# Optimization experiments

Hardware: AMD Instinct MI355X
Metric: run time of the kernel (lower is better)

## Reference

```python
import jax, jax.numpy as jnp
import numpy as np
import math

N_LEVELS = 16
F_PER_LEVEL = 2
LOG2_T = 19
T = 1 << LOG2_T
BASE_RES = 16
MAX_RES = 2048
PER_LEVEL_SCALE = (MAX_RES / BASE_RES) ** (1.0 / (N_LEVELS - 1))
BOUND = 0.5
PRIMES = (np.uint32(1), np.uint32(2654435761), np.uint32(805459861))


def _weight_norm(v, g):
    # w = g * v / ||v||_row (torch weight_norm over dim=1)
    return v * (g / jnp.linalg.norm(v, axis=1))[:, None]


def _softplus100(x):
    # torch Softplus(beta=100)
    return jax.nn.softplus(100.0 * x) * 0.01


def hashgrid_encode(x01, table):
    # x01: [N,3] in [0,1]; table: [L, T, F]
    feats = []
    for l in range(N_LEVELS):
        scale = BASE_RES * (PER_LEVEL_SCALE ** l) - 1.0  # tcnn grid scale
        res = int(math.ceil(scale)) + 1
        pos = x01 * scale + 0.5
        pos_floor = jnp.floor(pos)
        w = pos - pos_floor                      # [N,3] trilinear fracs
        c0 = pos_floor.astype(jnp.uint32)        # [N,3] base corner
        dense = (res ** 3) <= T                  # static per level
        acc = jnp.zeros((x01.shape[0], F_PER_LEVEL), dtype=table.dtype)
        for corner in range(8):
            off = [(corner >> d) & 1 for d in range(3)]
            cx = c0[:, 0] + np.uint32(off[0])
            cy = c0[:, 1] + np.uint32(off[1])
            cz = c0[:, 2] + np.uint32(off[2])
            if dense:
                idx = cx + cy * np.uint32(res) + cz * np.uint32(res * res)
            else:
                idx = (cx * PRIMES[0]) ^ (cy * PRIMES[1]) ^ (cz * PRIMES[2])
                idx = idx & np.uint32(T - 1)
            wc = ((w[:, 0] if off[0] else 1.0 - w[:, 0])
                  * (w[:, 1] if off[1] else 1.0 - w[:, 1])
                  * (w[:, 2] if off[2] else 1.0 - w[:, 2]))
            acc = acc + wc[:, None] * table[l, idx.astype(jnp.int32)]
        feats.append(acc)
    return jnp.concatenate(feats, axis=-1)  # [N, 32]


def setup_inputs() -> dict:
    key = jax.random.key(0)
    ks = jax.random.split(key, 4)
    N = 2 ** 21
    x = jax.random.uniform(ks[0], (N, 3), jnp.float32, -BOUND, BOUND)
    table = jax.random.uniform(ks[1], (N_LEVELS, T, F_PER_LEVEL), jnp.float32, -1e-4, 1e-4)
    d_in, d_hid, d_out = 35, 64, 13
    v1 = jax.random.normal(ks[2], (d_hid, d_in), jnp.float32) * (math.sqrt(2) / math.sqrt(d_hid))
    v2 = jax.random.normal(ks[3], (d_out, d_hid), jnp.float32) * 1e-4 + math.sqrt(math.pi) / math.sqrt(d_hid)
    g1 = jnp.linalg.norm(v1, axis=1)
    g2 = jnp.linalg.norm(v2, axis=1)
    b1 = jnp.zeros((d_hid,), jnp.float32)
    b2 = jnp.full((d_out,), -0.5, jnp.float32)  # -sphere_init_radius
    return {"x": x, "table": table, "v1": v1, "g1": g1, "b1": b1,
            "v2": v2, "g2": g2, "b2": b2}


def reference(x, table, v1, g1, b1, v2, g2, b2):
    x01 = jnp.clip((x + BOUND) / (2.0 * BOUND), 0.0, 1.0)
    enc = hashgrid_encode(x01, table)            # [N, 32]
    h = jnp.concatenate([x, enc], axis=1)        # [N, 35]
    w1 = _weight_norm(v1, g1)
    w2 = _weight_norm(v2, g2)
    h = _softplus100(h @ w1.T + b1)
    out = h @ w2.T + b2                          # [N, 13]
    return out
```

## Files before the change

kernel.cpp:

```cpp
#include <hip/hip_runtime.h>
#include <hip/hip_fp16.h>
#include <cstdint>
#include <cmath>

#define NLEV 16
#define NHASH 11
#define NDENSE 5
#define TBL (1u << 19)

struct LevelParams {
    float scale[NLEV];
    uint32_t res[NLEV];
    uint32_t hashed_mask;
};

__global__ __launch_bounds__(128) void prep_weights(
    const float* __restrict__ v1, const float* __restrict__ g1,
    const float* __restrict__ v2, const float* __restrict__ g2,
    float* __restrict__ w1t, float* __restrict__ w2n)
{
    int t = threadIdx.x;
    if (t < 64) {
        float s = 0.f;
        #pragma unroll
        for (int k = 0; k < 35; ++k) { float v = v1[t*35 + k]; s += v*v; }
        float f = g1[t] / sqrtf(s);
        #pragma unroll
        for (int k = 0; k < 35; ++k) w1t[k*64 + t] = v1[t*35 + k] * f;
    } else if (t < 77) {
        int r = t - 64;
        float s = 0.f;
        #pragma unroll
        for (int k = 0; k < 64; ++k) { float v = v2[r*64 + k]; s += v*v; }
        float f = g2[r] / sqrtf(s);
        #pragma unroll
        for (int k = 0; k < 64; ++k) w2n[r*64 + k] = v2[r*64 + k] * f;
    }
}

__global__ __launch_bounds__(256) void pack_table(
    const float2* __restrict__ in, uint32_t* __restrict__ out, int n)
{
    int i = blockIdx.x * 256 + threadIdx.x;
    if (i < n) {
        float2 v = in[i];
        __half2 h = __floats2half2_rn(v.x, v.y);
        out[i] = *reinterpret_cast<uint32_t*>(&h);
    }
}

__device__ __forceinline__ void encode_one(
    float u0, float u1, float u2, float s, uint32_t res, bool hashed,
    const uint32_t* __restrict__ tl, float& a0, float& a1)
{
    float px = u0 * s + 0.5f;
    float py = u1 * s + 0.5f;
    float pz = u2 * s + 0.5f;
    float fx = floorf(px), fy = floorf(py), fz = floorf(pz);
    float wx1 = px - fx, wy1 = py - fy, wz1 = pz - fz;
    float wx0 = 1.f - wx1, wy0 = 1.f - wy1, wz0 = 1.f - wz1;
    uint32_t cx = (uint32_t)fx, cy = (uint32_t)fy, cz = (uint32_t)fz;

    uint32_t ix0, ix1, iy0, iy1, iz0, iz1;
    if (hashed) {
        ix0 = cx;                 ix1 = cx + 1u;
        iy0 = cy * 2654435761u;   iy1 = (cy + 1u) * 2654435761u;
        iz0 = cz * 805459861u;    iz1 = (cz + 1u) * 805459861u;
    } else {
        ix0 = cx;                 ix1 = cx + 1u;
        iy0 = cy * res;           iy1 = iy0 + res;
        uint32_t rr = res * res;
        iz0 = cz * rr;            iz1 = iz0 + rr;
    }

    uint32_t idxs[8];
    #pragma unroll
    for (int c = 0; c < 8; ++c) {
        uint32_t jx = (c & 1) ? ix1 : ix0;
        uint32_t jy = (c & 2) ? iy1 : iy0;
        uint32_t jz = (c & 4) ? iz1 : iz0;
        idxs[c] = hashed ? ((jx ^ jy ^ jz) & (TBL - 1u)) : (jx + jy + jz);
    }
    uint32_t raw[8];
    #pragma unroll
    for (int c = 0; c < 8; ++c) raw[c] = tl[idxs[c]];

    float wxy00 = wx0*wy0, wxy10 = wx1*wy0, wxy01 = wx0*wy1, wxy11 = wx1*wy1;
    a0 = 0.f; a1 = 0.f;
    #pragma unroll
    for (int c = 0; c < 8; ++c) {
        float wxy = (c & 2) ? ((c & 1) ? wxy11 : wxy01)
                            : ((c & 1) ? wxy10 : wxy00);
        float w = wxy * ((c & 4) ? wz1 : wz0);
        __half2 hv = *reinterpret_cast<__half2*>(&raw[c]);
        float2 v = __half22float2(hv);
        a0 += w * v.x;
        a1 += w * v.y;
    }
}

__global__ __launch_bounds__(256) void encode_hashed(
    const float* __restrict__ x, const uint32_t* __restrict__ tpk,
    uint32_t* __restrict__ feats, int N, int chunks_per_level, LevelParams P)
{
    int bid = blockIdx.x;
    int li = bid / chunks_per_level;
    int l = li + NDENSE;
    int base = (bid - li * chunks_per_level) * 512 + threadIdx.x;
    const uint32_t* tl = tpk + (size_t)l * TBL;
    float s = P.scale[l];

    int p[2] = { base, base + 256 };

    uint2 Q[2][4];
    uint32_t par[2];
    float wx0[2], wx1[2], wyz[2][4];

    #pragma unroll
    for (int t = 0; t < 2; ++t) {
        int pp = (p[t] < N) ? p[t] : (N - 1);
        float x0 = __builtin_nontemporal_load(&x[3*(size_t)pp + 0]);
        float x1 = __builtin_nontemporal_load(&x[3*(size_t)pp + 1]);
        float x2 = __builtin_nontemporal_load(&x[3*(size_t)pp + 2]);
        float u0 = fminf(fmaxf(x0 + 0.5f, 0.f), 1.f);
        float u1 = fminf(fmaxf(x1 + 0.5f, 0.f), 1.f);
        float u2 = fminf(fmaxf(x2 + 0.5f, 0.f), 1.f);

        float px = u0 * s + 0.5f;
        float py = u1 * s + 0.5f;
        float pz = u2 * s + 0.5f;
        float fx = floorf(px), fy = floorf(py), fz = floorf(pz);
        float a1f = px - fx, b1f = py - fy, c1f = pz - fz;
        wx1[t] = a1f; wx0[t] = 1.f - a1f;
        float wy0 = 1.f - b1f, wz0 = 1.f - c1f;
        uint32_t cx = (uint32_t)fx, cy = (uint32_t)fy, cz = (uint32_t)fz;

        wyz[t][0] = wy0 * wz0;
        wyz[t][1] = b1f * wz0;
        wyz[t][2] = wy0 * c1f;
        wyz[t][3] = b1f * c1f;

        uint32_t hy0 = cy * 2654435761u, hy1 = (cy + 1u) * 2654435761u;
        uint32_t hz0 = cz * 805459861u,  hz1 = (cz + 1u) * 805459861u;
        uint32_t r[4] = { hy0 ^ hz0, hy1 ^ hz0, hy0 ^ hz1, hy1 ^ hz1 };

        par[t] = 0u;
        if (!(cx & 1u)) {
            #pragma unroll
            for (int k = 0; k < 4; ++k) {
                uint32_t v0 = (cx ^ r[k]) & (TBL - 1u);
                Q[t][k] = *reinterpret_cast<const uint2*>(tl + (v0 & ~1u));
                par[t] |= (v0 & 1u) << k;
            }
        } else {
            #pragma unroll
            for (int k = 0; k < 4; ++k) {
                uint32_t v0 = (cx ^ r[k]) & (TBL - 1u);
                uint32_t v1 = ((cx + 1u) ^ r[k]) & (TBL - 1u);
                Q[t][k].x = tl[v0];
                Q[t][k].y = tl[v1];
            }
        }
    }

    #pragma unroll
    for (int t = 0; t < 2; ++t) {
        float a0 = 0.f, a1 = 0.f;
        #pragma unroll
        for (int k = 0; k < 4; ++k) {
            uint32_t swap = (par[t] >> k) & 1u;
            uint32_t b0 = swap ? Q[t][k].y : Q[t][k].x;
            uint32_t b1 = swap ? Q[t][k].x : Q[t][k].y;
            __half2 h0 = *reinterpret_cast<__half2*>(&b0);
            __half2 h1 = *reinterpret_cast<__half2*>(&b1);
            float2 c0 = __half22float2(h0);
            float2 c1 = __half22float2(h1);
            a0 += wyz[t][k] * (wx0[t] * c0.x + wx1[t] * c1.x);
            a1 += wyz[t][k] * (wx0[t] * c0.y + wx1[t] * c1.y);
        }
        __half2 hv = __floats2half2_rn(a0, a1);
        if (p[t] < N) {
            __builtin_nontemporal_store(*reinterpret_cast<uint32_t*>(&hv),
                                        &feats[(size_t)li * N + p[t]]);
        }
    }
}

__global__ __launch_bounds__(256) void mlp_dense(
    const float* __restrict__ x, const uint32_t* __restrict__ tpk,
    const uint32_t* __restrict__ feats,
    const float* __restrict__ w1t,
    const float* __restrict__ b1,
    const float* __restrict__ w2,
    const float* __restrict__ b2,
    float* __restrict__ out, int N, LevelParams P)
{
    int p = blockIdx.x * 256 + threadIdx.x;
    bool valid = (p < N);
    int pp = valid ? p : (N - 1);

    float x0 = x[3*(size_t)pp + 0];
    float x1 = x[3*(size_t)pp + 1];
    float x2 = x[3*(size_t)pp + 2];
    float u0 = fminf(fmaxf(x0 + 0.5f, 0.f), 1.f);
    float u1 = fminf(fmaxf(x1 + 0.5f, 0.f), 1.f);
    float u2 = fminf(fmaxf(x2 + 0.5f, 0.f), 1.f);

    uint32_t rf[NHASH];
    #pragma unroll
    for (int li = 0; li < NHASH; ++li) rf[li] = feats[(size_t)li * N + pp];

    float h[64];
    #pragma unroll
    for (int j = 0; j < 64; ++j) {
        h[j] = b1[j] + x0 * w1t[0*64 + j] + x1 * w1t[1*64 + j] + x2 * w1t[2*64 + j];
    }

    #pragma unroll
    for (int l = 0; l < NDENSE; ++l) {
        const uint32_t* tl = tpk + (size_t)l * TBL;
        float a0, a1;
        encode_one(u0, u1, u2, P.scale[l], P.res[l], false, tl, a0, a1);
        const float* c0p = w1t + (3 + 2*l) * 64;
        const float* c1p = c0p + 64;
        #pragma unroll
        for (int j = 0; j < 64; ++j) h[j] += a0 * c0p[j] + a1 * c1p[j];
    }

    #pragma unroll
    for (int li = 0; li < NHASH; ++li) {
        __half2 hv = *reinterpret_cast<__half2*>(&rf[li]);
        float2 f = __half22float2(hv);
        int l = li + NDENSE;
        const float* c0p = w1t + (3 + 2*l) * 64;
        const float* c1p = c0p + 64;
        #pragma unroll
        for (int j = 0; j < 64; ++j) h[j] += f.x * c0p[j] + f.y * c1p[j];
    }

    #pragma unroll
    for (int j = 0; j < 64; ++j) {
        float z = 100.f * h[j];
        float t = __expf(-fabsf(z));
        h[j] = (fmaxf(z, 0.f) + __logf(1.f + t)) * 0.01f;
    }

    float* op = out + (size_t)pp * 13;
    for (int o = 0; o < 13; ++o) {
        float a = b2[o];
        const float* wr = w2 + o * 64;
        #pragma unroll
        for (int k = 0; k < 64; ++k) a = fmaf(h[k], wr[k], a);
        if (valid) op[o] = a;
    }
}

template <int PACKED>
__global__ __launch_bounds__(256) void sdf_fused(
    const float* __restrict__ x, const void* __restrict__ table,
    const float* __restrict__ w1t, const float* __restrict__ b1,
    const float* __restrict__ w2, const float* __restrict__ b2,
    float* __restrict__ out, int N, LevelParams P)
{
    int i = blockIdx.x * 256 + threadIdx.x;
    bool valid = (i < N);
    int ii = valid ? i : (N - 1);

    float x0 = x[3*(size_t)ii + 0];
    float x1 = x[3*(size_t)ii + 1];
    float x2 = x[3*(size_t)ii + 2];
    float u0 = fminf(fmaxf(x0 + 0.5f, 0.f), 1.f);
    float u1 = fminf(fmaxf(x1 + 0.5f, 0.f), 1.f);
    float u2 = fminf(fmaxf(x2 + 0.5f, 0.f), 1.f);

    float h[64];
    #pragma unroll
    for (int j = 0; j < 64; ++j) {
        h[j] = b1[j] + x0 * w1t[0*64 + j] + x1 * w1t[1*64 + j] + x2 * w1t[2*64 + j];
    }

    for (int l = 0; l < NLEV; ++l) {
        bool hashed = (P.hashed_mask >> l) & 1u;
        float a0, a1;
        if (PACKED) {
            const uint32_t* tl = (const uint32_t*)table + (size_t)l * TBL;
            encode_one(u0, u1, u2, P.scale[l], P.res[l], hashed, tl, a0, a1);
        } else {
            const float* tl = (const float*)table + (size_t)l * (size_t)(TBL * 2u);
            float s = P.scale[l]; uint32_t res = P.res[l];
            float px = u0*s + 0.5f, py = u1*s + 0.5f, pz = u2*s + 0.5f;
            float fx = floorf(px), fy = floorf(py), fz = floorf(pz);
            float wx1 = px-fx, wy1 = py-fy, wz1 = pz-fz;
            float wx0 = 1.f-wx1, wy0 = 1.f-wy1, wz0 = 1.f-wz1;
            uint32_t cx = (uint32_t)fx, cy = (uint32_t)fy, cz = (uint32_t)fz;
            a0 = 0.f; a1 = 0.f;
            #pragma unroll
            for (int c = 0; c < 8; ++c) {
                uint32_t jx = cx + (c & 1);
                uint32_t jy = cy + ((c >> 1) & 1);
                uint32_t jz = cz + ((c >> 2) & 1);
                uint32_t idx = hashed
                    ? ((jx ^ (jy * 2654435761u) ^ (jz * 805459861u)) & (TBL - 1u))
                    : (jx + jy * res + jz * res * res);
                float w = ((c & 1) ? wx1 : wx0) * ((c & 2) ? wy1 : wy0)
                        * ((c & 4) ? wz1 : wz0);
                float2 v = *reinterpret_cast<const float2*>(tl + (size_t)idx * 2u);
                a0 += w * v.x; a1 += w * v.y;
            }
        }
        const float* c0p = w1t + (3 + 2*l) * 64;
        const float* c1p = c0p + 64;
        #pragma unroll
        for (int j = 0; j < 64; ++j) h[j] += a0 * c0p[j] + a1 * c1p[j];
    }

    #pragma unroll
    for (int j = 0; j < 64; ++j) {
        float z = 100.f * h[j];
        float t = __expf(-fabsf(z));
        h[j] = (fmaxf(z, 0.f) + __logf(1.f + t)) * 0.01f;
    }

    float* op = out + (size_t)ii * 13;
    for (int o = 0; o < 13; ++o) {
        float a = b2[o];
        const float* wr = w2 + o * 64;
        #pragma unroll
        for (int k = 0; k < 64; ++k) a += h[k] * wr[k];
        if (valid) op[o] = a;
    }
}

extern "C" void kernel_launch(void* const* d_in, const int* in_sizes, int n_in,
                              void* d_out, int out_size, void* d_ws, size_t ws_size,
                              hipStream_t stream)
{
    const float* x     = (const float*)d_in[0];
    const float* table = (const float*)d_in[1];
    const float* v1    = (const float*)d_in[2];
    const float* g1    = (const float*)d_in[3];
    const float* b1    = (const float*)d_in[4];
    const float* v2    = (const float*)d_in[5];
    const float* g2    = (const float*)d_in[6];
    const float* b2    = (const float*)d_in[7];
    float* out = (float*)d_out;
    int N = in_sizes[0] / 3;

    const int n_entries = NLEV * (int)TBL;
    const size_t packed_bytes = (size_t)n_entries * 4u;
    const size_t feats_bytes  = (size_t)NHASH * (size_t)N * 4u;
    const size_t w_bytes = (35*64 + 13*64) * sizeof(float);

    bool two_pass  = (ws_size >= packed_bytes + feats_bytes + w_bytes);
    bool packed_ok = (ws_size >= packed_bytes + w_bytes);

    uint32_t* tpk   = (uint32_t*)d_ws;
    uint32_t* feats = (uint32_t*)((char*)d_ws + packed_bytes);
    size_t w_off = packed_ok ? (packed_bytes + (two_pass ? feats_bytes : 0)) : 0;
    float* w1t = (float*)((char*)d_ws + w_off);
    float* w2n = w1t + 35 * 64;

    LevelParams P;
    P.hashed_mask = 0u;
    double pls = pow(128.0, 1.0 / 15.0);
    for (int l = 0; l < NLEV; ++l) {
        double sc = 16.0 * pow(pls, (double)l) - 1.0;
        P.scale[l] = (float)sc;
        uint32_t res = (uint32_t)(ceil(sc)) + 1u;
        P.res[l] = res;
        uint64_t r3 = (uint64_t)res * res * res;
        if (r3 > (uint64_t)TBL) P.hashed_mask |= (1u << l);
    }

    prep_weights<<<1, 128, 0, stream>>>(v1, g1, v2, g2, w1t, w2n);

    int chunks = (N + 255) / 256;
    if (two_pass) {
        pack_table<<<(n_entries + 255) / 256, 256, 0, stream>>>(
            (const float2*)table, tpk, n_entries);
        int chunks2 = (N + 511) / 512;
        encode_hashed<<<chunks2 * NHASH, 256, 0, stream>>>(
            x, tpk, feats, N, chunks2, P);
        mlp_dense<<<chunks, 256, 0, stream>>>(
            x, tpk, feats, w1t, b1, w2n, b2, out, N, P);
    } else if (packed_ok) {
        pack_table<<<(n_entries + 255) / 256, 256, 0, stream>>>(
            (const float2*)table, tpk, n_entries);
        sdf_fused<1><<<chunks, 256, 0, stream>>>(
            x, (const void*)tpk, w1t, b1, w2n, b2, out, N, P);
    } else {
        sdf_fused<0><<<chunks, 256, 0, stream>>>(
            x, (const void*)table, w1t, b1, w2n, b2, out, N, P);
    }
}
```

Baseline: 780.5 us.

## Spatially bucket-sort points before hash-grid encoding to improve gather locality

Adds a counting sort of points into a 32^3 spatial grid (histogram, scan, atomic scatter) that writes packed float4 coordinates with the original index. The encode and MLP kernels then read the sorted points, and outputs are scattered back to their original positions. The aim is to make table gathers from neighbouring threads hit nearby entries so cache hit rates improve for the random uniform inputs. In exchange it adds extra kernels, global atomics, a 32 MB sorted buffer and scattered output writes, and it runs only when the workspace is large enough.

```diff
diff --git a/kernel.cpp b/kernel.cpp
--- a/kernel.cpp
+++ b/kernel.cpp
@@ -7,6 +7,7 @@
 #define NHASH 11
 #define NDENSE 5
 #define TBL (1u << 19)
+#define NBKT 32768
 
 struct LevelParams {
     float scale[NLEV];
@@ -46,6 +47,75 @@
         float2 v = in[i];
         __half2 h = __floats2half2_rn(v.x, v.y);
         out[i] = *reinterpret_cast<uint32_t*>(&h);
+    }
+}
+
+__device__ __forceinline__ uint32_t bucket_key(float u0, float u1, float u2)
+{
+    uint32_t a = min(31u, (uint32_t)(u0 * 32.f));
+    uint32_t b = min(31u, (uint32_t)(u1 * 32.f));
+    uint32_t c = min(31u, (uint32_t)(u2 * 32.f));
+    return (a << 10) | (b << 5) | c;
+}
+
+__device__ __forceinline__ void load_u(const float* __restrict__ x, int pp,
+                                       float& u0, float& u1, float& u2)
+{
+    float x0 = x[3*(size_t)pp + 0];
+    float x1 = x[3*(size_t)pp + 1];
+    float x2 = x[3*(size_t)pp + 2];
+    u0 = fminf(fmaxf(x0 + 0.5f, 0.f), 1.f);
+    u1 = fminf(fmaxf(x1 + 0.5f, 0.f), 1.f);
+    u2 = fminf(fmaxf(x2 + 0.5f, 0.f), 1.f);
+}
+
+__global__ __launch_bounds__(256) void hist_kernel(
+    const float* __restrict__ x, uint32_t* __restrict__ hist, int N)
+{
+    int i = blockIdx.x * 256 + threadIdx.x;
+    if (i < N) {
+        float u0, u1, u2;
+        load_u(x, i, u0, u1, u2);
+        atomicAdd(&hist[bucket_key(u0, u1, u2)], 1u);
+    }
+}
+
+__global__ __launch_bounds__(1024) void scan_hist(
+    const uint32_t* __restrict__ hist, uint32_t* __restrict__ offs)
+{
+    __shared__ uint32_t part[1024];
+    int t = threadIdx.x;
+    uint32_t loc[32];
+    uint32_t s = 0;
+    #pragma unroll
+    for (int k = 0; k < 32; ++k) { loc[k] = s; s += hist[t*32 + k]; }
+    part[t] = s;
+    __syncthreads();
+    for (int d = 1; d < 1024; d <<= 1) {
+        uint32_t v = (t >= d) ? part[t - d] : 0u;
+        __syncthreads();
+        part[t] += v;
+        __syncthreads();
+    }
+    uint32_t base = (t > 0) ? part[t - 1] : 0u;
+    #pragma unroll
+    for (int k = 0; k < 32; ++k) offs[t*32 + k] = base + loc[k];
+}
+
+__global__ __launch_bounds__(256) void scatter_kernel(
+    const float* __restrict__ x, uint32_t* __restrict__ offs,
+    float4* __restrict__ xs4, int N)
+{
+    int i = blockIdx.x * 256 + threadIdx.x;
+    if (i < N) {
+        float x0 = x[3*(size_t)i + 0];
+        float x1 = x[3*(size_t)i + 1];
+        float x2 = x[3*(size_t)i + 2];
+        float u0 = fminf(fmaxf(x0 + 0.5f, 0.f), 1.f);
+        float u1 = fminf(fmaxf(x1 + 0.5f, 0.f), 1.f);
+        float u2 = fminf(fmaxf(x2 + 0.5f, 0.f), 1.f);
+        uint32_t pos = atomicAdd(&offs[bucket_key(u0, u1, u2)], 1u);
+        xs4[pos] = make_float4(x0, x1, x2, __int_as_float(i));
     }
 }
 
@@ -99,8 +169,10 @@
     }
 }
 
+template <int SORTED>
 __global__ __launch_bounds__(256) void encode_hashed(
-    const float* __restrict__ x, const uint32_t* __restrict__ tpk,
+    const float* __restrict__ x, const float4* __restrict__ xs4,
+    const uint32_t* __restrict__ tpk,
     uint32_t* __restrict__ feats, int N, int chunks_per_level, LevelParams P)
 {
     int bid = blockIdx.x;
@@ -119,12 +191,15 @@
     #pragma unroll
     for (int t = 0; t < 2; ++t) {
         int pp = (p[t] < N) ? p[t] : (N - 1);
-        float x0 = __builtin_nontemporal_load(&x[3*(size_t)pp + 0]);
-        float x1 = __builtin_nontemporal_load(&x[3*(size_t)pp + 1]);
-        float x2 = __builtin_nontemporal_load(&x[3*(size_t)pp + 2]);
-        float u0 = fminf(fmaxf(x0 + 0.5f, 0.f), 1.f);
-        float u1 = fminf(fmaxf(x1 + 0.5f, 0.f), 1.f);
-        float u2 = fminf(fmaxf(x2 + 0.5f, 0.f), 1.f);
+        float u0, u1, u2;
+        if (SORTED) {
+            float4 v4 = xs4[pp];
+            u0 = fminf(fmaxf(v4.x + 0.5f, 0.f), 1.f);
+            u1 = fminf(fmaxf(v4.y + 0.5f, 0.f), 1.f);
+            u2 = fminf(fmaxf(v4.z + 0.5f, 0.f), 1.f);
+        } else {
+            load_u(x, pp, u0, u1, u2);
+        }
 
         float px = u0 * s + 0.5f;
         float py = u1 * s + 0.5f;
@@ -186,8 +261,10 @@
     }
 }
 
+template <int SORTED>
 __global__ __launch_bounds__(256) void mlp_dense(
-    const float* __restrict__ x, const uint32_t* __restrict__ tpk,
+    const float* __restrict__ x, const float4* __restrict__ xs4,
+    const uint32_t* __restrict__ tpk,
     const uint32_t* __restrict__ feats,
     const float* __restrict__ w1t,
     const float* __restrict__ b1,
@@ -199,9 +276,18 @@
     bool valid = (p < N);
     int pp = valid ? p : (N - 1);
 
-    float x0 = x[3*(size_t)pp + 0];
-    float x1 = x[3*(size_t)pp + 1];
-    float x2 = x[3*(size_t)pp + 2];
+    float x0, x1, x2;
+    int oidx;
+    if (SORTED) {
+        float4 v4 = xs4[pp];
+        x0 = v4.x; x1 = v4.y; x2 = v4.z;
+        oidx = __float_as_int(v4.w);
+    } else {
+        x0 = x[3*(size_t)pp + 0];
+        x1 = x[3*(size_t)pp + 1];
+        x2 = x[3*(size_t)pp + 2];
+        oidx = pp;
+    }
     float u0 = fminf(fmaxf(x0 + 0.5f, 0.f), 1.f);
     float u1 = fminf(fmaxf(x1 + 0.5f, 0.f), 1.f);
     float u2 = fminf(fmaxf(x2 + 0.5f, 0.f), 1.f);
@@ -245,7 +331,7 @@
         h[j] = (fmaxf(z, 0.f) + __logf(1.f + t)) * 0.01f;
     }
 
-    float* op = out + (size_t)pp * 13;
+    float* op = out + (size_t)oidx * 13;
     for (int o = 0; o < 13; ++o) {
         float a = b2[o];
         const float* wr = w2 + o * 64;
@@ -266,12 +352,13 @@
     bool valid = (i < N);
     int ii = valid ? i : (N - 1);
 
+    float u0, u1, u2;
     float x0 = x[3*(size_t)ii + 0];
     float x1 = x[3*(size_t)ii + 1];
     float x2 = x[3*(size_t)ii + 2];
-    float u0 = fminf(fmaxf(x0 + 0.5f, 0.f), 1.f);
-    float u1 = fminf(fmaxf(x1 + 0.5f, 0.f), 1.f);
-    float u2 = fminf(fmaxf(x2 + 0.5f, 0.f), 1.f);
+    u0 = fminf(fmaxf(x0 + 0.5f, 0.f), 1.f);
+    u1 = fminf(fmaxf(x1 + 0.5f, 0.f), 1.f);
+    u2 = fminf(fmaxf(x2 + 0.5f, 0.f), 1.f);
 
     float h[64];
     #pragma unroll
@@ -348,16 +435,39 @@
 
     const int n_entries = NLEV * (int)TBL;
     const size_t packed_bytes = (size_t)n_entries * 4u;
+    const size_t xs4_bytes    = (size_t)N * 16u;
     const size_t feats_bytes  = (size_t)NHASH * (size_t)N * 4u;
+    const size_t hist_bytes   = (size_t)NBKT * 4u;
     const size_t w_bytes = (35*64 + 13*64) * sizeof(float);
 
+    size_t off_packed = 0;
+    size_t off_xs4    = off_packed + packed_bytes;
+    size_t off_feats  = off_xs4 + xs4_bytes;
+    size_t off_hist   = off_feats + feats_bytes;
+    size_t off_offs   = off_hist + hist_bytes;
+    size_t off_w      = off_offs + hist_bytes;
+    size_t sorted_need = off_w + w_bytes;
+
+    bool sorted_ok = (ws_size >= sorted_need);
     bool two_pass  = (ws_size >= packed_bytes + feats_bytes + w_bytes);
     bool packed_ok = (ws_size >= packed_bytes + w_bytes);
 
-    uint32_t* tpk   = (uint32_t*)d_ws;
-    uint32_t* feats = (uint32_t*)((char*)d_ws + packed_bytes);
-    size_t w_off = packed_ok ? (packed_bytes + (two_pass ? feats_bytes : 0)) : 0;
-    float* w1t = (float*)((char*)d_ws + w_off);
+    uint32_t* tpk   = (uint32_t*)((char*)d_ws + off_packed);
+    float4*   xs4   = (float4*)((char*)d_ws + off_xs4);
+    uint32_t* feats;
+    uint32_t* hist  = (uint32_t*)((char*)d_ws + off_hist);
+    uint32_t* offs  = (uint32_t*)((char*)d_ws + off_offs);
+    float* w1t;
+    if (sorted_ok) {
+        feats = (uint32_t*)((char*)d_ws + off_feats);
+        w1t = (float*)((char*)d_ws + off_w);
+    } else if (two_pass) {
+        feats = (uint32_t*)((char*)d_ws + packed_bytes);
+        w1t = (float*)((char*)d_ws + packed_bytes + feats_bytes);
+    } else {
+        feats = nullptr;
+        w1t = (float*)((char*)d_ws + (packed_ok ? packed_bytes : 0));
+    }
     float* w2n = w1t + 35 * 64;
 
     LevelParams P;
@@ -375,14 +485,26 @@
     prep_weights<<<1, 128, 0, stream>>>(v1, g1, v2, g2, w1t, w2n);
 
     int chunks = (N + 255) / 256;
-    if (two_pass) {
+    if (sorted_ok) {
+        pack_table<<<(n_entries + 255) / 256, 256, 0, stream>>>(
+            (const float2*)table, tpk, n_entries);
+        hipMemsetAsync(hist, 0, hist_bytes, stream);
+        hist_kernel<<<chunks, 256, 0, stream>>>(x, hist, N);
+        scan_hist<<<1, 1024, 0, stream>>>(hist, offs);
+        scatter_kernel<<<chunks, 256, 0, stream>>>(x, offs, xs4, N);
+        int chunks2 = (N + 511) / 512;
+        encode_hashed<1><<<chunks2 * NHASH, 256, 0, stream>>>(
+            x, xs4, tpk, feats, N, chunks2, P);
+        mlp_dense<1><<<chunks, 256, 0, stream>>>(
+            x, xs4, tpk, feats, w1t, b1, w2n, b2, out, N, P);
+    } else if (two_pass) {
         pack_table<<<(n_entries + 255) / 256, 256, 0, stream>>>(
             (const float2*)table, tpk, n_entries);
         int chunks2 = (N + 511) / 512;
-        encode_hashed<<<chunks2 * NHASH, 256, 0, stream>>>(
-            x, tpk, feats, N, chunks2, P);
-        mlp_dense<<<chunks, 256, 0, stream>>>(
-            x, tpk, feats, w1t, b1, w2n, b2, out, N, P);
+        encode_hashed<0><<<chunks2 * NHASH, 256, 0, stream>>>(
+            x, nullptr, tpk, feats, N, chunks2, P);
+        mlp_dense<0><<<chunks, 256, 0, stream>>>(
+            x, nullptr, tpk, feats, w1t, b1, w2n, b2, out, N, P);
     } else if (packed_ok) {
         pack_table<<<(n_entries + 255) / 256, 256, 0, stream>>>(
             (const float2*)table, tpk, n_entries);
```

New measurement: 865.9 us. 10.9% more time.
